# Performance work log

Measured on AMD Instinct MI355X. Metric: run time of the kernel, lower is better.

## Reference

```python
import jax, jax.numpy as jnp
import numpy as np

VMF_KAPPA = 30.0      # vMF concentration
THRESHOLD = 0.0       # vc_thresholds
OCC_LIKELY = 0.6      # occ_likely[0]
NUM_MIXTURES = 4
EPS_L1 = 1e-12        # torch F.normalize eps


def _l1_normalize(x, axis):
    n = jnp.sum(jnp.abs(x), axis=axis, keepdims=True)
    return x / jnp.maximum(n, EPS_L1)


def _crop_or_pad(mm, H, W):
    # center crop or zero-pad mix model spatial dims to (H, W); shapes are static
    _, _, hm, wm = mm.shape
    if hm < H:
        d1 = (H - hm) // 2
        mm = jnp.pad(mm, ((0, 0), (0, 0), (d1, H - hm - d1), (0, 0)))
    elif hm > H:
        d1 = (hm - H) // 2
        mm = mm[:, :, d1:d1 + H, :]
    if wm < W:
        d1 = (W - wm) // 2
        mm = jnp.pad(mm, ((0, 0), (0, 0), (0, 0), (d1, W - wm - d1)))
    elif wm > W:
        d1 = (wm - W) // 2
        mm = mm[:, :, :, d1:d1 + W]
    return mm


def setup_inputs() -> dict:
    key = jax.random.key(0)
    k1, k2, k3, k4 = jax.random.split(key, 4)
    B, C, H, W = 32, 512, 56, 56
    VC = 512              # number of vMF codebook vectors
    KM = 48               # num_classes(12) * num_mixtures(4)
    NCLUT = 5             # clutter models
    return {
        "vgg_feat": jax.random.normal(k1, (B, C, H, W), dtype=jnp.float32),
        "conv_weight": jax.random.normal(k2, (VC, C, 1, 1), dtype=jnp.float32),
        "mix_model": jax.random.uniform(k3, (KM, VC, H, W), dtype=jnp.float32),
        "clutter_model": jax.random.uniform(k4, (NCLUT, VC), dtype=jnp.float32),
    }


def reference(vgg_feat, conv_weight, mix_model, clutter_model):
    B, C, H, W = vgg_feat.shape
    # --- Conv1o1: cosine similarity between L2-normalized features and codebook ---
    xnorm = jnp.linalg.norm(vgg_feat, axis=1, keepdims=True)
    xnorm = xnorm + (xnorm == 0).astype(vgg_feat.dtype)  # avoid div-by-zero
    xn = vgg_feat / xnorm
    w = conv_weight[:, :, 0, 0]                           # (vc, C) 1x1 kernel
    wn = w / jnp.linalg.norm(w, axis=1, keepdims=True)
    cos = jnp.einsum('bchw,kc->bkhw', xn, wn)             # (B, vc, H, W)
    # --- vMF activation ---
    act = jnp.exp(VMF_KAPPA * cos) * (cos > THRESHOLD).astype(cos.dtype)
    # --- PointwiseInferenceLayer (vmf, use_mixture_bg=True) ---
    ck = _l1_normalize(jnp.clip(clutter_model, 0.0, 1.0), axis=1)  # (N, vc)
    bg = jnp.einsum('bkhw,nk->bnhw', act, ck)                      # (B, N, H, W)
    background = jnp.log(bg * OCC_LIKELY + 1e-10)
    background = jnp.max(background, axis=1, keepdims=True)        # (B, 1, H, W)
    background = background[:, None, None]                         # (B,1,1,1,H,W)

    mm = _l1_normalize(jnp.clip(mix_model, 0.0, 1.0), axis=1)      # (KM, vc, Hm, Wm)
    mm = _crop_or_pad(mm, H, W)
    fg = jnp.einsum('bkhw,mkhw->bmhw', act, mm)                    # (B, KM, H, W)
    foreground = jnp.log(fg * (1.0 - OCC_LIKELY) + 1e-10)
    num_classes = mm.shape[0] // NUM_MIXTURES
    foreground = foreground.reshape(B, num_classes, NUM_MIXTURES, 1, H, W)
    per_model = jnp.maximum(foreground, background).sum(axis=(-1, -2))  # (B,K,M,1)
    scores = per_model.max(axis=-1).max(axis=-1)                        # (B, K)
    mix_likeli = scores / (H * W)
    # SoftMaxTemp(2.0)
    z = jnp.exp(jnp.clip(mix_likeli * 2.0, -88.7, 88.7))
    soft = z / jnp.sum(z, axis=1, keepdims=True)
    return soft, vgg_feat, mix_likeli
```

## Files before the change

kernel.cpp:

```cpp
#include <hip/hip_runtime.h>

#define B_ 32
#define C_ 512
#define HW_ 3136
#define KF_ 512
#define KM_ 48
#define NCL_ 5

typedef __attribute__((ext_vector_type(8))) short short8;
typedef __attribute__((ext_vector_type(4))) short short4v;
typedef __attribute__((ext_vector_type(4))) float floatx4;
typedef unsigned int u32;
typedef u32 __attribute__((address_space(1))) gu32;
typedef u32 __attribute__((address_space(3))) lu32;

__device__ __forceinline__ unsigned short f2bf(float f) {
    union { float f; unsigned u; } v; v.f = f;
    unsigned r = v.u + 0x7FFFu + ((v.u >> 16) & 1u);
    return (unsigned short)(r >> 16);
}
__device__ __forceinline__ float bf2f(unsigned short u) {
    union { unsigned u; float f; } v; v.u = ((unsigned)u) << 16;
    return v.f;
}
__device__ __forceinline__ void gl2lds16(const void* g, void* l) {
    __builtin_amdgcn_global_load_lds((const gu32*)g, (lu32*)l, 16, 0, 0);
}
__device__ __forceinline__ void gl2lds4(const void* g, void* l) {
    __builtin_amdgcn_global_load_lds((const gu32*)g, (lu32*)l, 4, 0, 0);
}

__global__ __launch_bounds__(64) void prep_kernel(const float* __restrict__ w,
                                                  const float* __restrict__ cl,
                                                  unsigned short* __restrict__ wn,
                                                  unsigned short* __restrict__ ckb) {
    int bid = blockIdx.x, t = threadIdx.x;
    if (bid < KF_) {
        const float* row = w + (size_t)bid * C_;
        float ss = 0.f;
        float x[8];
#pragma unroll
        for (int j = 0; j < 8; ++j) { x[j] = row[t * 8 + j]; ss += x[j] * x[j]; }
        for (int m = 32; m >= 1; m >>= 1) ss += __shfl_xor(ss, m);
        float inv = 1.f / sqrtf(ss);
#pragma unroll
        for (int j = 0; j < 8; ++j) wn[(size_t)bid * C_ + t * 8 + j] = f2bf(x[j] * inv);
    } else {
        int n = bid - KF_;
        if (n >= 16) return;
        if (n < NCL_) {
            const float* row = cl + (size_t)n * KF_;
            float s = 0.f;
            float v[8];
#pragma unroll
            for (int j = 0; j < 8; ++j) {
                float x = row[t * 8 + j];
                x = fminf(fmaxf(x, 0.f), 1.f);
                v[j] = x; s += x;
            }
            for (int m = 32; m >= 1; m >>= 1) s += __shfl_xor(s, m);
            float inv = 1.f / fmaxf(s, 1e-12f);
#pragma unroll
            for (int j = 0; j < 8; ++j) ckb[(size_t)n * KF_ + t * 8 + j] = f2bf(v[j] * inv);
        } else {
#pragma unroll
            for (int j = 0; j < 8; ++j) ckb[(size_t)n * KF_ + t * 8 + j] = 0;
        }
    }
}

__global__ __launch_bounds__(512) void xprep_kernel(const float* __restrict__ vgg,
                                                    unsigned short* __restrict__ xnt,
                                                    float* __restrict__ invn,
                                                    float* __restrict__ out_vgg,
                                                    int write_vgg) {
    int pt = blockIdx.x, b = blockIdx.y;
    int tid = threadIdx.x;
    int px = tid & 63, cq = tid >> 6;
    __shared__ __align__(16) unsigned short tile[64][512];
    __shared__ float ssp[8][64];
    const float* vcol = vgg + (size_t)b * C_ * HW_ + pt * 64 + px;
    float* ovcol = out_vgg + (size_t)b * C_ * HW_ + pt * 64 + px;

    float ss = 0.f;
#pragma unroll
    for (int j = 0; j < 16; ++j) {
        int c0 = cq * 64 + j * 4;
        float x0 = vcol[(size_t)(c0 + 0) * HW_];
        float x1 = vcol[(size_t)(c0 + 1) * HW_];
        float x2 = vcol[(size_t)(c0 + 2) * HW_];
        float x3 = vcol[(size_t)(c0 + 3) * HW_];
        ss += x0 * x0 + x1 * x1 + x2 * x2 + x3 * x3;
        short4v pk;
        pk[0] = (short)f2bf(x0); pk[1] = (short)f2bf(x1);
        pk[2] = (short)f2bf(x2); pk[3] = (short)f2bf(x3);
        *(short4v*)&tile[px][c0] = pk;
        if (write_vgg) {
            ovcol[(size_t)(c0 + 0) * HW_] = x0;
            ovcol[(size_t)(c0 + 1) * HW_] = x1;
            ovcol[(size_t)(c0 + 2) * HW_] = x2;
            ovcol[(size_t)(c0 + 3) * HW_] = x3;
        }
    }
    ssp[cq][px] = ss;
    __syncthreads();
    if (tid < 64) {
        float s = 0.f;
#pragma unroll
        for (int q = 0; q < 8; ++q) s += ssp[q][tid];
        float n = sqrtf(s);
        invn[(size_t)b * HW_ + pt * 64 + tid] = (n == 0.f) ? 1.f : 1.f / n;
    }
    __syncthreads();
    int row = tid >> 3, ch = tid & 7;
    unsigned short* orow = xnt + ((size_t)b * HW_ + pt * 64 + row) * 512;
#pragma unroll
    for (int j = 0; j < 8; ++j) {
        int c8 = (ch + 8 * j) * 8;
        *(short8*)(orow + c8) = *(const short8*)&tile[row][c8];
    }
}

__global__ __launch_bounds__(512) void gemm_act_kernel(const unsigned short* __restrict__ xnt,
                                                       const unsigned short* __restrict__ wn,
                                                       const float* __restrict__ invn,
                                                       unsigned short* __restrict__ act) {
    int wg = blockIdx.x;
    int swz = (wg & 7) * 392 + (wg >> 3);
    int pt = swz >> 2, ft = swz & 3;
    int tid = threadIdx.x, lane = tid & 63;
    int wid = tid >> 6;
    int li = lane & 15, q = lane >> 4;
    int wm = wid & 1, wq = wid >> 1;

    __shared__ __align__(16) unsigned short a_lds[2][128 * 64];
    __shared__ __align__(16) unsigned short b_lds[2][128 * 64];
    __shared__ float inv_l[128];
    if (tid < 128) inv_l[tid] = invn[(size_t)pt * 128 + tid];

    const unsigned short* ga = wn + ((size_t)ft * 128 + (tid >> 3)) * 512 + (tid & 7) * 8;
    const unsigned short* gb = xnt + ((size_t)pt * 128 + (tid >> 3)) * 512 + (tid & 7) * 8;
    int ldst = tid * 8;

    floatx4 acc[4][2] = {};

#pragma unroll
    for (int i = 0; i < 2; ++i) {
        gl2lds16(ga + (size_t)i * 64 * 512, &a_lds[0][ldst + i * 4096]);
        gl2lds16(gb + (size_t)i * 64 * 512, &b_lds[0][ldst + i * 4096]);
    }
    __syncthreads();

#pragma unroll 1
    for (int s = 0; s < 8; ++s) {
        if (s < 7) {
            int nb = (s + 1) & 1;
#pragma unroll
            for (int i = 0; i < 2; ++i) {
                gl2lds16(ga + (size_t)i * 64 * 512 + (s + 1) * 64, &a_lds[nb][ldst + i * 4096]);
                gl2lds16(gb + (size_t)i * 64 * 512 + (s + 1) * 64, &b_lds[nb][ldst + i * 4096]);
            }
        }
        int buf = s & 1;
#pragma unroll
        for (int k2 = 0; k2 < 2; ++k2) {
            short8 af[4], bfr[2];
#pragma unroll
            for (int i = 0; i < 4; ++i)
                af[i] = *(const short8*)&a_lds[buf][(wm * 64 + i * 16 + li) * 64 + k2 * 32 + q * 8];
#pragma unroll
            for (int j = 0; j < 2; ++j)
                bfr[j] = *(const short8*)&b_lds[buf][(wq * 32 + j * 16 + li) * 64 + k2 * 32 + q * 8];
#pragma unroll
            for (int i = 0; i < 4; ++i)
#pragma unroll
                for (int j = 0; j < 2; ++j)
                    acc[i][j] = __builtin_amdgcn_mfma_f32_16x16x32_bf16(af[i], bfr[j], acc[i][j], 0, 0, 0);
        }
        __syncthreads();
    }

#pragma unroll
    for (int j = 0; j < 2; ++j) {
        int px = wq * 32 + j * 16 + li;
        float inv = inv_l[px];
        size_t row_g = (size_t)pt * 128 + px;
#pragma unroll
        for (int i = 0; i < 4; ++i) {
            int chn = ft * 8 + wm * 4 + i;
            short4v pk;
#pragma unroll
            for (int r = 0; r < 4; ++r) {
                float cv = acc[i][j][r] * inv;
                float a = cv > 0.f ? __expf(30.f * cv) : 0.f;
                pk[r] = (short)f2bf(a);
            }
            *(short4v*)(act + ((size_t)chn * 100352 + row_g) * 16 + q * 4) = pk;
        }
    }
}

#define MMBUF 50112
#define ACTBUF 16640
#define OFF_ACT0 (2*MMBUF)
#define OFF_CSUM (2*MMBUF + 2*ACTBUF)
#define OFF_PMS  (OFF_CSUM + 3072)
#define OFF_CKB  (OFF_PMS + 6144)
__global__ __launch_bounds__(1024) void fg_kernel(const unsigned short* __restrict__ act,
                                                  const float* __restrict__ mm,
                                                  const unsigned short* __restrict__ ckb,
                                                  float* __restrict__ pm) {
    __shared__ __align__(16) unsigned char L[OFF_CKB + 16 * 520 * 2];
    float* csum_s = (float*)(L + OFF_CSUM);
    float* pms    = (float*)(L + OFF_PMS);
    unsigned short* ckbl = (unsigned short*)(L + OFF_CKB);

    int p0 = blockIdx.x * 16;
    int tid = threadIdx.x;
    int lane = tid & 63, wid = tid >> 6;
    int li = lane & 15, q = lane >> 4;
    int pp = wid;
    int w3 = wid * 3;

    for (int i = tid; i < 1536; i += 1024) pms[i] = 0.f;
    {
        int row = tid >> 6, cg = tid & 63;
        *(short8*)&ckbl[row * 520 + cg * 8] = *(const short8*)(ckb + row * 512 + cg * 8);
    }

    const float* mm_src = mm + ((size_t)(w3 * KF_) + (size_t)(lane >> 4)) * HW_ + p0 + (lane & 15);
    const unsigned short* act_src = act +
        ((size_t)(2 * wid + (lane >> 5)) * HW_ + p0 + ((lane >> 1) & 15)) * 16 + (lane & 1) * 8;

    auto stage = [&](int s) {
        unsigned char* mb = L + (s & 1) * MMBUF;
        unsigned char* ab = L + OFF_ACT0 + (s & 1) * ACTBUF;
        const float* ms = mm_src + (size_t)s * 16 * HW_;
#pragma unroll
        for (int jj = 0; jj < 12; ++jj)
            gl2lds4(ms + (size_t)((jj >> 2) * KF_ + (jj & 3) * 4) * HW_,
                    mb + (w3 + (jj >> 2)) * 1044 + (jj & 3) * 256);
        gl2lds16(act_src + (size_t)s * 100352 * 16, ab + wid * 1040);
    };

    short8 fa[2] = {};
    short8 fmA[3] = {};
    short8 fck = {};
    floatx4 acc[3][2] = {};
    floatx4 accbg[2] = {};
    float csp[3] = {0.f, 0.f, 0.f};

    stage(0);
    __syncthreads();

#pragma unroll 2
    for (int s = 0; s < 32; ++s) {
        if (s < 31) stage(s + 1);
        const unsigned char* mc = L + (s & 1) * MMBUF;
        const unsigned char* ac = L + OFF_ACT0 + (s & 1) * ACTBUF;
        if ((q >> 1) == (s & 1)) {
#pragma unroll
            for (int bf = 0; bf < 2; ++bf)
                fa[bf] = *(const short8*)(ac + (bf * 8 + (li >> 1)) * 1040 +
                                          ((li & 1) * 16 + pp) * 32 + (q & 1) * 16);
#pragma unroll
            for (int mf = 0; mf < 3; ++mf) {
                const unsigned char* arow = mc + (mf * 16 + li) * 1044 + (q & 1) * 512 + pp * 4;
                short8 pk;
                float s0 = 0.f;
#pragma unroll
                for (int j = 0; j < 8; ++j) {
                    float x = *(const float*)(arow + j * 64);
                    x = fminf(fmaxf(x, 0.f), 1.f);
                    s0 += x;
                    pk[j] = (short)f2bf(x);
                }
                csp[mf] += s0;
                fmA[mf] = pk;
            }
            fck = *(const short8*)&ckbl[li * 520 + s * 16 + (q & 1) * 8];
        }
        if (s & 1) {
#pragma unroll
            for (int mf = 0; mf < 3; ++mf) {
                acc[mf][0] = __builtin_amdgcn_mfma_f32_16x16x32_bf16(fmA[mf], fa[0], acc[mf][0], 0, 0, 0);
                acc[mf][1] = __builtin_amdgcn_mfma_f32_16x16x32_bf16(fmA[mf], fa[1], acc[mf][1], 0, 0, 0);
            }
            accbg[0] = __builtin_amdgcn_mfma_f32_16x16x32_bf16(fck, fa[0], accbg[0], 0, 0, 0);
            accbg[1] = __builtin_amdgcn_mfma_f32_16x16x32_bf16(fck, fa[1], accbg[1], 0, 0, 0);
        }
        __syncthreads();
    }

#pragma unroll
    for (int mf = 0; mf < 3; ++mf) {
        float v = csp[mf];
        v += __shfl_xor(v, 16);
        v += __shfl_xor(v, 32);
        if (q == 0) csum_s[(mf * 16 + li) * 16 + pp] = v;
    }

    float bgv[2];
#pragma unroll
    for (int bf = 0; bf < 2; ++bf) {
        float v = -1e30f;
#pragma unroll
        for (int r = 0; r < 4; ++r) v = fmaxf(v, logf(accbg[bf][r] * 0.6f + 1e-10f));
        v = fmaxf(v, __shfl_xor(v, 16));
        v = fmaxf(v, __shfl_xor(v, 32));
        bgv[bf] = v;
    }
    __syncthreads();

#pragma unroll
    for (int mf = 0; mf < 3; ++mf)
#pragma unroll
        for (int bf = 0; bf < 2; ++bf) {
            int b = bf * 16 + li;
#pragma unroll
            for (int r = 0; r < 4; ++r) {
                int m = mf * 16 + q * 4 + r;
                float inv = 1.f / fmaxf(csum_s[m * 16 + pp], 1e-12f);
                float v = fmaxf(logf(acc[mf][bf][r] * inv * 0.4f + 1e-10f), bgv[bf]);
                atomicAdd(&pms[m * 32 + b], v);
            }
        }
    __syncthreads();
    if (tid < 512) {
        int i3 = tid * 3;
#pragma unroll
        for (int j = 0; j < 3; ++j) {
            int i = i3 + j;
            int m = i >> 5, b = i & 31;
            atomicAdd(&pm[(size_t)b * KM_ + m], pms[i]);
        }
    }
}

__global__ __launch_bounds__(64) void final_kernel(const float* __restrict__ pm,
                                                   float* __restrict__ out_soft,
                                                   float* __restrict__ out_ml) {
    int b = threadIdx.x;
    if (b >= B_) return;
    float ml[12];
#pragma unroll
    for (int c = 0; c < 12; ++c) {
        float s = -1e30f;
#pragma unroll
        for (int j = 0; j < 4; ++j) s = fmaxf(s, pm[(size_t)b * KM_ + c * 4 + j]);
        ml[c] = s / (float)HW_;
    }
    float z[12], zs = 0.f;
#pragma unroll
    for (int c = 0; c < 12; ++c) {
        float e = fminf(fmaxf(ml[c] * 2.f, -88.7f), 88.7f);
        z[c] = expf(e); zs += z[c];
    }
#pragma unroll
    for (int c = 0; c < 12; ++c) {
        out_soft[(size_t)b * 12 + c] = z[c] / zs;
        out_ml[(size_t)b * 12 + c] = ml[c];
    }
}

extern "C" void kernel_launch(void* const* d_in, const int* in_sizes, int n_in,
                              void* d_out, int out_size, void* d_ws, size_t ws_size,
                              hipStream_t stream) {
    const float* vgg = (const float*)d_in[0];
    const float* cw  = (const float*)d_in[1];
    const float* mmp = (const float*)d_in[2];
    const float* cl  = (const float*)d_in[3];
    float* out = (float*)d_out;
    char* ws = (char*)d_ws;

    unsigned short* wn   = (unsigned short*)(ws);
    unsigned short* ckb  = (unsigned short*)(ws + 524288);
    float* invn          = (float*)(ws + 540672);
    float* pm            = (float*)(ws + 942080);
    unsigned short* xnt  = (unsigned short*)(ws + 948224);
    const size_t ACT_OFF = 948224 + 102760448;
    const size_t ACT_BYTES = (size_t)B_ * HW_ * KF_ * 2;

    int big_ws = (ws_size >= ACT_OFF + ACT_BYTES) ? 1 : 0;
    unsigned short* act = big_ws ? (unsigned short*)(ws + ACT_OFF)
                                 : (unsigned short*)(out + 384);

    hipMemsetAsync(pm, 0, (size_t)B_ * KM_ * sizeof(float), stream);
    prep_kernel<<<dim3(KF_ + 16), dim3(64), 0, stream>>>(cw, cl, wn, ckb);
    xprep_kernel<<<dim3(49, 32), dim3(512), 0, stream>>>(vgg, xnt, invn, out + 384, big_ws);
    gemm_act_kernel<<<dim3(3136), dim3(512), 0, stream>>>(xnt, wn, invn, act);
    fg_kernel<<<dim3(196), dim3(1024), 0, stream>>>(act, mmp, ckb, pm);
    final_kernel<<<1, 64, 0, stream>>>(pm, out, out + 384 + (size_t)B_ * C_ * HW_);
    if (!big_ws)
        hipMemcpyAsync(out + 384, vgg, (size_t)B_ * C_ * HW_ * sizeof(float),
                       hipMemcpyDeviceToDevice, stream);
}
```

Baseline: 405.9 us.

## Pre-convert mix model to bf16 and add triple-buffered foreground MFMA kernel

Adds a prep kernel that clamps the fp32 mix model, converts it to bf16 in a blocked layout, and writes per-pixel channel sums. A new 512-thread foreground kernel consumes this with a 3-stage async global-to-LDS pipeline and explicit vmcnt waits. It replaces the old kernel, which read and normalized fp32 mix-model data inline. The GEMM kernel also swaps __syncthreads for raw barriers with partial vmcnt waits so loads overlap compute. The new path needs a much larger workspace and falls back to the old path if that is not available.

After: 448.1 us. 1.1x slower.

```diff
diff --git a/kernel.cpp b/kernel.cpp
--- a/kernel.cpp
+++ b/kernel.cpp
@@ -121,6 +121,36 @@
     }
 }
 
+__global__ __launch_bounds__(448) void mmprep_kernel(const float* __restrict__ mm,
+                                                     unsigned short* __restrict__ mmb,
+                                                     float* __restrict__ csumg) {
+    int m = blockIdx.x;
+    int kh = blockIdx.z;
+    int px = blockIdx.y * 448 + threadIdx.x;
+    const float* src = mm + ((size_t)m * KF_ + kh * 256) * HW_ + px;
+    unsigned short* dst = mmb + ((size_t)(m * 32 + kh * 16) * HW_ + px) * 16;
+    float cs = 0.f;
+#pragma unroll 1
+    for (int ch = 0; ch < 16; ++ch) {
+        short8 lo, hi;
+#pragma unroll
+        for (int kin = 0; kin < 8; ++kin) {
+            float x = src[(size_t)(ch * 16 + kin) * HW_];
+            x = fminf(fmaxf(x, 0.f), 1.f);
+            cs += x; lo[kin] = (short)f2bf(x);
+        }
+#pragma unroll
+        for (int kin = 8; kin < 16; ++kin) {
+            float x = src[(size_t)(ch * 16 + kin) * HW_];
+            x = fminf(fmaxf(x, 0.f), 1.f);
+            cs += x; hi[kin - 8] = (short)f2bf(x);
+        }
+        *(short8*)(dst + (size_t)ch * HW_ * 16) = lo;
+        *(short8*)(dst + (size_t)ch * HW_ * 16 + 8) = hi;
+    }
+    csumg[(size_t)kh * 48 * HW_ + (size_t)m * HW_ + px] = cs;
+}
+
 __global__ __launch_bounds__(512) void gemm_act_kernel(const unsigned short* __restrict__ xnt,
                                                        const unsigned short* __restrict__ wn,
                                                        const float* __restrict__ invn,
@@ -149,10 +179,10 @@
         gl2lds16(ga + (size_t)i * 64 * 512, &a_lds[0][ldst + i * 4096]);
         gl2lds16(gb + (size_t)i * 64 * 512, &b_lds[0][ldst + i * 4096]);
     }
-    __syncthreads();
 
 #pragma unroll 1
     for (int s = 0; s < 8; ++s) {
+        __builtin_amdgcn_s_barrier();
         if (s < 7) {
             int nb = (s + 1) & 1;
 #pragma unroll
@@ -160,7 +190,12 @@
                 gl2lds16(ga + (size_t)i * 64 * 512 + (s + 1) * 64, &a_lds[nb][ldst + i * 4096]);
                 gl2lds16(gb + (size_t)i * 64 * 512 + (s + 1) * 64, &b_lds[nb][ldst + i * 4096]);
             }
-        }
+            asm volatile("s_waitcnt vmcnt(4)" ::: "memory");
+        } else {
+            asm volatile("s_waitcnt vmcnt(0)" ::: "memory");
+        }
+        __builtin_amdgcn_sched_barrier(0);
+        __builtin_amdgcn_s_barrier();
         int buf = s & 1;
 #pragma unroll
         for (int k2 = 0; k2 < 2; ++k2) {
@@ -177,7 +212,6 @@
                 for (int j = 0; j < 2; ++j)
                     acc[i][j] = __builtin_amdgcn_mfma_f32_16x16x32_bf16(af[i], bfr[j], acc[i][j], 0, 0, 0);
         }
-        __syncthreads();
     }
 
 #pragma unroll
@@ -196,6 +230,148 @@
                 pk[r] = (short)f2bf(a);
             }
             *(short4v*)(act + ((size_t)chn * 100352 + row_g) * 16 + q * 4) = pk;
+        }
+    }
+}
+
+#define FG_ABUF 16640
+#define FG_MBUF 24960
+#define FG_BUF  (FG_ABUF + FG_MBUF)
+#define FG_OFF_CSUM (3 * FG_BUF)
+#define FG_OFF_PMS  (FG_OFF_CSUM + 3072)
+#define FG_OFF_CKB  (FG_OFF_PMS + 6144)
+__global__ __launch_bounds__(512) void fg2_kernel(const unsigned short* __restrict__ act,
+                                                  const unsigned short* __restrict__ mmb,
+                                                  const float* __restrict__ csumg,
+                                                  const unsigned short* __restrict__ ckb,
+                                                  float* __restrict__ pm) {
+    __shared__ __align__(16) unsigned char L[150656];
+    float* csum_s = (float*)(L + FG_OFF_CSUM);
+    float* pms    = (float*)(L + FG_OFF_PMS);
+    unsigned short* ckbl = (unsigned short*)(L + FG_OFF_CKB);
+
+    int p0 = blockIdx.x * 16;
+    int tid = threadIdx.x;
+    int lane = tid & 63, w = tid >> 6;
+    int li = lane & 15, q = lane >> 4;
+
+    for (int i = tid; i < 1536; i += 512) pms[i] = 0.f;
+    for (int i = tid; i < 768; i += 512) {
+        int m = i >> 4, pp = i & 15;
+        size_t idx = (size_t)m * HW_ + p0 + pp;
+        csum_s[i] = csumg[idx] + csumg[(size_t)48 * HW_ + idx];
+    }
+    {
+        int row = tid >> 5, cg = tid & 31;
+        *(short8*)&ckbl[row * 520 + cg * 16] = *(const short8*)(ckb + row * 512 + cg * 16);
+        *(short8*)&ckbl[row * 520 + cg * 16 + 8] = *(const short8*)(ckb + row * 512 + cg * 16 + 8);
+    }
+    __syncthreads();
+
+    size_t a_lane = ((size_t)(lane >> 5) * HW_ + p0 + ((lane >> 1) & 15)) * 16 + (lane & 1) * 8;
+    size_t m_lane = (size_t)(lane >> 5) * 1605632 + ((size_t)p0 + ((lane >> 1) & 15)) * 16 + (lane & 1) * 8;
+
+    auto stage = [&](int s) {
+        unsigned char* ab = L + (s % 3) * FG_BUF;
+        unsigned char* mb = ab + FG_ABUF;
+        const unsigned short* as = act + (size_t)s * 1605632 + a_lane;
+        const unsigned short* ms = mmb + (size_t)s * 50176 + m_lane;
+#pragma unroll
+        for (int t = 0; t < 2; ++t) {
+            int j = w + t * 8;
+            gl2lds16(as + (size_t)(2 * j) * (HW_ * 16), ab + j * 1040);
+        }
+#pragma unroll
+        for (int t = 0; t < 3; ++t) {
+            int j = w + t * 8;
+            gl2lds16(ms + (size_t)(2 * j) * 1605632, mb + j * 1040);
+        }
+    };
+
+    short8 fa[2][2] = {};
+    short8 fm[2][3] = {};
+    short8 fck = {};
+    floatx4 acc[2][3][2] = {};
+    floatx4 abg[2][2] = {};
+
+    stage(0);
+    stage(1);
+
+#pragma unroll 2
+    for (int s = 0; s < 32; ++s) {
+        __builtin_amdgcn_s_barrier();
+        if (s < 30) {
+            stage(s + 2);
+            asm volatile("s_waitcnt vmcnt(10)" ::: "memory");
+        } else if (s == 30) {
+            asm volatile("s_waitcnt vmcnt(5)" ::: "memory");
+        } else {
+            asm volatile("s_waitcnt vmcnt(0)" ::: "memory");
+        }
+        __builtin_amdgcn_sched_barrier(0);
+        __builtin_amdgcn_s_barrier();
+        const unsigned char* ab = L + (s % 3) * FG_BUF;
+        const unsigned char* mb = ab + FG_ABUF;
+        if ((q >> 1) == (s & 1)) {
+#pragma unroll
+            for (int e = 0; e < 2; ++e) {
+                int pp = w * 2 + e;
+#pragma unroll
+                for (int bf = 0; bf < 2; ++bf)
+                    fa[e][bf] = *(const short8*)(ab + (bf * 8 + (li >> 1)) * 1040 +
+                                                 ((li & 1) * 16 + pp) * 32 + (q & 1) * 16);
+#pragma unroll
+                for (int mf = 0; mf < 3; ++mf)
+                    fm[e][mf] = *(const short8*)(mb + (mf * 8 + (li >> 1)) * 1040 +
+                                                 ((li & 1) * 16 + pp) * 32 + (q & 1) * 16);
+            }
+            fck = *(const short8*)&ckbl[li * 520 + s * 16 + (q & 1) * 8];
+        }
+        if (s & 1) {
+#pragma unroll
+            for (int e = 0; e < 2; ++e) {
+#pragma unroll
+                for (int mf = 0; mf < 3; ++mf) {
+                    acc[e][mf][0] = __builtin_amdgcn_mfma_f32_16x16x32_bf16(fm[e][mf], fa[e][0], acc[e][mf][0], 0, 0, 0);
+                    acc[e][mf][1] = __builtin_amdgcn_mfma_f32_16x16x32_bf16(fm[e][mf], fa[e][1], acc[e][mf][1], 0, 0, 0);
+                }
+                abg[e][0] = __builtin_amdgcn_mfma_f32_16x16x32_bf16(fck, fa[e][0], abg[e][0], 0, 0, 0);
+                abg[e][1] = __builtin_amdgcn_mfma_f32_16x16x32_bf16(fck, fa[e][1], abg[e][1], 0, 0, 0);
+            }
+        }
+    }
+
+#pragma unroll
+    for (int e = 0; e < 2; ++e) {
+        int pp = w * 2 + e;
+#pragma unroll
+        for (int bf = 0; bf < 2; ++bf) {
+            int b = bf * 16 + li;
+            float v = -1e30f;
+#pragma unroll
+            for (int r = 0; r < 4; ++r) v = fmaxf(v, logf(abg[e][bf][r] * 0.6f + 1e-10f));
+            v = fmaxf(v, __shfl_xor(v, 16));
+            v = fmaxf(v, __shfl_xor(v, 32));
+            float bgv = v;
+#pragma unroll
+            for (int mf = 0; mf < 3; ++mf)
+#pragma unroll
+                for (int r = 0; r < 4; ++r) {
+                    int m = mf * 16 + q * 4 + r;
+                    float inv = 1.f / fmaxf(csum_s[m * 16 + pp], 1e-12f);
+                    float fv = fmaxf(logf(acc[e][mf][bf][r] * inv * 0.4f + 1e-10f), bgv);
+                    atomicAdd(&pms[m * 32 + b], fv);
+                }
+        }
+    }
+    __syncthreads();
+    {
+        int i3 = tid * 3;
+#pragma unroll
+        for (int j = 0; j < 3; ++j) {
+            int i = i3 + j;
+            int m = i >> 5, b = i & 31;
+            atomicAdd(&pm[(size_t)b * KM_ + m], pms[i]);
         }
     }
 }
@@ -206,10 +382,10 @@
 #define OFF_CSUM (2*MMBUF + 2*ACTBUF)
 #define OFF_PMS  (OFF_CSUM + 3072)
 #define OFF_CKB  (OFF_PMS + 6144)
-__global__ __launch_bounds__(1024) void fg_kernel(const unsigned short* __restrict__ act,
-                                                  const float* __restrict__ mm,
-                                                  const unsigned short* __restrict__ ckb,
-                                                  float* __restrict__ pm) {
+__global__ __launch_bounds__(1024) void fg_fb_kernel(const unsigned short* __restrict__ act,
+                                                     const float* __restrict__ mm,
+                                                     const unsigned short* __restrict__ ckb,
+                                                     float* __restrict__ pm) {
     __shared__ __align__(16) unsigned char L[OFF_CKB + 16 * 520 * 2];
     float* csum_s = (float*)(L + OFF_CSUM);
     float* pms    = (float*)(L + OFF_PMS);
@@ -377,21 +553,39 @@
     unsigned short* ckb  = (unsigned short*)(ws + 524288);
     float* invn          = (float*)(ws + 540672);
     float* pm            = (float*)(ws + 942080);
-    unsigned short* xnt  = (unsigned short*)(ws + 948224);
-    const size_t ACT_OFF = 948224 + 102760448;
+    float* csumg         = (float*)(ws + 948224);
+    unsigned short* xnt  = (unsigned short*)(ws + 2152448);
+    unsigned short* mmb  = (unsigned short*)(ws + 104912896);
+    const size_t MID_NEED = 104912896ull + 154140672ull;
     const size_t ACT_BYTES = (size_t)B_ * HW_ * KF_ * 2;
-
-    int big_ws = (ws_size >= ACT_OFF + ACT_BYTES) ? 1 : 0;
-    unsigned short* act = big_ws ? (unsigned short*)(ws + ACT_OFF)
-                                 : (unsigned short*)(out + 384);
 
     hipMemsetAsync(pm, 0, (size_t)B_ * KM_ * sizeof(float), stream);
     prep_kernel<<<dim3(KF_ + 16), dim3(64), 0, stream>>>(cw, cl, wn, ckb);
-    xprep_kernel<<<dim3(49, 32), dim3(512), 0, stream>>>(vgg, xnt, invn, out + 384, big_ws);
-    gemm_act_kernel<<<dim3(3136), dim3(512), 0, stream>>>(xnt, wn, invn, act);
-    fg_kernel<<<dim3(196), dim3(1024), 0, stream>>>(act, mmp, ckb, pm);
-    final_kernel<<<1, 64, 0, stream>>>(pm, out, out + 384 + (size_t)B_ * C_ * HW_);
-    if (!big_ws)
-        hipMemcpyAsync(out + 384, vgg, (size_t)B_ * C_ * HW_ * sizeof(float),
-                       hipMemcpyDeviceToDevice, stream);
-}
+
+    if (ws_size >= MID_NEED) {
+        int act_in_ws = (ws_size >= MID_NEED + ACT_BYTES) ? 1 : 0;
+        unsigned short* act = act_in_ws ? (unsigned short*)(ws + MID_NEED)
+                                        : (unsigned short*)(out + 384);
+        xprep_kernel<<<dim3(49, 32), dim3(512), 0, stream>>>(vgg, xnt, invn, out + 384, act_in_ws);
+        mmprep_kernel<<<dim3(48, 7, 2), dim3(448), 0, stream>>>(mmp, mmb, csumg);
+        gemm_act_kernel<<<dim3(3136), dim3(512), 0, stream>>>(xnt, wn, invn, act);
+        fg2_kernel<<<dim3(196), dim3(512), 0, stream>>>(act, mmb, csumg, ckb, pm);
+        final_kernel<<<1, 64, 0, stream>>>(pm, out, out + 384 + (size_t)B_ * C_ * HW_);
+        if (!act_in_ws)
+            hipMemcpyAsync(out + 384, vgg, (size_t)B_ * C_ * HW_ * sizeof(float),
+                           hipMemcpyDeviceToDevice, stream);
+    } else {
+        unsigned short* xnt2 = (unsigned short*)(ws + 948224);
+        const size_t ACT_OFF = 948224 + 102760448;
+        int big_ws = (ws_size >= ACT_OFF + ACT_BYTES) ? 1 : 0;
+        unsigned short* act = big_ws ? (unsigned short*)(ws + ACT_OFF)
+                                     : (unsigned short*)(out + 384);
+        xprep_kernel<<<dim3(49, 32), dim3(512), 0, stream>>>(vgg, xnt2, invn, out + 384, big_ws);
+        gemm_act_kernel<<<dim3(3136), dim3(512), 0, stream>>>(xnt2, wn, invn, act);
+        fg_fb_kernel<<<dim3(196), dim3(1024), 0, stream>>>(act, mmp, ckb, pm);
+        final_kernel<<<1, 64, 0, stream>>>(pm, out, out + 384 + (size_t)B_ * C_ * HW_);
+        if (!big_ws)
+            hipMemcpyAsync(out + 384, vgg, (size_t)B_ * C_ * HW_ * sizeof(float),
+                           hipMemcpyDeviceToDevice, stream);
+    }
+}
```

## Fuse background clutter reduction into GEMM epilogue and retile foreground kernel

Applied to the files above, without the earlier changes.

Moves the clutter-model background dot product into the GEMM epilogue, accumulating per-pixel fp32 sums through shared-memory and global atomics into a new workspace buffer. This removes the background MFMA work from the foreground kernel. The foreground kernel is rewritten as fg3 with 64-pixel by 16-mixture tiles, XOR-swizzled LDS layouts and a 4-step register staging cycle. The GEMM main loop replaces __syncthreads with explicit vmcnt waits and split barriers. The cost is an extra memset, extra global atomics per pixel, and higher LDS use in the GEMM.

Result: slower. 451.9 us (+11.3%).

```diff
diff --git a/kernel.cpp b/kernel.cpp
--- a/kernel.cpp
+++ b/kernel.cpp
@@ -19,21 +19,14 @@
     unsigned r = v.u + 0x7FFFu + ((v.u >> 16) & 1u);
     return (unsigned short)(r >> 16);
 }
-__device__ __forceinline__ float bf2f(unsigned short u) {
-    union { unsigned u; float f; } v; v.u = ((unsigned)u) << 16;
-    return v.f;
-}
 __device__ __forceinline__ void gl2lds16(const void* g, void* l) {
     __builtin_amdgcn_global_load_lds((const gu32*)g, (lu32*)l, 16, 0, 0);
-}
-__device__ __forceinline__ void gl2lds4(const void* g, void* l) {
-    __builtin_amdgcn_global_load_lds((const gu32*)g, (lu32*)l, 4, 0, 0);
 }
 
 __global__ __launch_bounds__(64) void prep_kernel(const float* __restrict__ w,
                                                   const float* __restrict__ cl,
                                                   unsigned short* __restrict__ wn,
-                                                  unsigned short* __restrict__ ckb) {
+                                                  float* __restrict__ ck) {
     int bid = blockIdx.x, t = threadIdx.x;
     if (bid < KF_) {
         const float* row = w + (size_t)bid * C_;
@@ -47,25 +40,20 @@
         for (int j = 0; j < 8; ++j) wn[(size_t)bid * C_ + t * 8 + j] = f2bf(x[j] * inv);
     } else {
         int n = bid - KF_;
-        if (n >= 16) return;
-        if (n < NCL_) {
-            const float* row = cl + (size_t)n * KF_;
-            float s = 0.f;
-            float v[8];
-#pragma unroll
-            for (int j = 0; j < 8; ++j) {
-                float x = row[t * 8 + j];
-                x = fminf(fmaxf(x, 0.f), 1.f);
-                v[j] = x; s += x;
-            }
-            for (int m = 32; m >= 1; m >>= 1) s += __shfl_xor(s, m);
-            float inv = 1.f / fmaxf(s, 1e-12f);
-#pragma unroll
-            for (int j = 0; j < 8; ++j) ckb[(size_t)n * KF_ + t * 8 + j] = f2bf(v[j] * inv);
-        } else {
-#pragma unroll
-            for (int j = 0; j < 8; ++j) ckb[(size_t)n * KF_ + t * 8 + j] = 0;
-        }
+        if (n >= NCL_) return;
+        const float* row = cl + (size_t)n * KF_;
+        float s = 0.f;
+        float v[8];
+#pragma unroll
+        for (int j = 0; j < 8; ++j) {
+            float x = row[t * 8 + j];
+            x = fminf(fmaxf(x, 0.f), 1.f);
+            v[j] = x; s += x;
+        }
+        for (int m = 32; m >= 1; m >>= 1) s += __shfl_xor(s, m);
+        float inv = 1.f / fmaxf(s, 1e-12f);
+#pragma unroll
+        for (int j = 0; j < 8; ++j) ck[(size_t)n * KF_ + t * 8 + j] = v[j] * inv;
     }
 }
 
@@ -124,7 +112,9 @@
 __global__ __launch_bounds__(512) void gemm_act_kernel(const unsigned short* __restrict__ xnt,
                                                        const unsigned short* __restrict__ wn,
                                                        const float* __restrict__ invn,
-                                                       unsigned short* __restrict__ act) {
+                                                       const float* __restrict__ ck,
+                                                       unsigned short* __restrict__ act,
+                                                       float* __restrict__ bgacc) {
     int wg = blockIdx.x;
     int swz = (wg & 7) * 392 + (wg >> 3);
     int pt = swz >> 2, ft = swz & 3;
@@ -136,7 +126,11 @@
     __shared__ __align__(16) unsigned short a_lds[2][128 * 64];
     __shared__ __align__(16) unsigned short b_lds[2][128 * 64];
     __shared__ float inv_l[128];
+    __shared__ float ck_l[NCL_ * KF_];
+    __shared__ float bga_l[128 * NCL_];
     if (tid < 128) inv_l[tid] = invn[(size_t)pt * 128 + tid];
+    for (int i = tid; i < NCL_ * KF_; i += 512) ck_l[i] = ck[i];
+    for (int i = tid; i < 128 * NCL_; i += 512) bga_l[i] = 0.f;
 
     const unsigned short* ga = wn + ((size_t)ft * 128 + (tid >> 3)) * 512 + (tid & 7) * 8;
     const unsigned short* gb = xnt + ((size_t)pt * 128 + (tid >> 3)) * 512 + (tid & 7) * 8;
@@ -149,10 +143,10 @@
         gl2lds16(ga + (size_t)i * 64 * 512, &a_lds[0][ldst + i * 4096]);
         gl2lds16(gb + (size_t)i * 64 * 512, &b_lds[0][ldst + i * 4096]);
     }
-    __syncthreads();
 
 #pragma unroll 1
     for (int s = 0; s < 8; ++s) {
+        __builtin_amdgcn_s_barrier();
         if (s < 7) {
             int nb = (s + 1) & 1;
 #pragma unroll
@@ -160,7 +154,12 @@
                 gl2lds16(ga + (size_t)i * 64 * 512 + (s + 1) * 64, &a_lds[nb][ldst + i * 4096]);
                 gl2lds16(gb + (size_t)i * 64 * 512 + (s + 1) * 64, &b_lds[nb][ldst + i * 4096]);
             }
-        }
+            asm volatile("s_waitcnt vmcnt(4)" ::: "memory");
+        } else {
+            asm volatile("s_waitcnt vmcnt(0)" ::: "memory");
+        }
+        __builtin_amdgcn_sched_barrier(0);
+        __builtin_amdgcn_s_barrier();
         int buf = s & 1;
 #pragma unroll
         for (int k2 = 0; k2 < 2; ++k2) {
@@ -177,7 +176,6 @@
                 for (int j = 0; j < 2; ++j)
                     acc[i][j] = __builtin_amdgcn_mfma_f32_16x16x32_bf16(af[i], bfr[j], acc[i][j], 0, 0, 0);
         }
-        __syncthreads();
     }
 
 #pragma unroll
@@ -185,155 +183,189 @@
         int px = wq * 32 + j * 16 + li;
         float inv = inv_l[px];
         size_t row_g = (size_t)pt * 128 + px;
+        float bp[NCL_] = {0.f, 0.f, 0.f, 0.f, 0.f};
 #pragma unroll
         for (int i = 0; i < 4; ++i) {
             int chn = ft * 8 + wm * 4 + i;
+            int f_g = ft * 128 + wm * 64 + i * 16 + q * 4;
             short4v pk;
+            float av[4];
 #pragma unroll
             for (int r = 0; r < 4; ++r) {
                 float cv = acc[i][j][r] * inv;
                 float a = cv > 0.f ? __expf(30.f * cv) : 0.f;
+                av[r] = a;
                 pk[r] = (short)f2bf(a);
             }
             *(short4v*)(act + ((size_t)chn * 100352 + row_g) * 16 + q * 4) = pk;
-        }
-    }
-}
-
-#define MMBUF 50112
-#define ACTBUF 16640
-#define OFF_ACT0 (2*MMBUF)
-#define OFF_CSUM (2*MMBUF + 2*ACTBUF)
-#define OFF_PMS  (OFF_CSUM + 3072)
-#define OFF_CKB  (OFF_PMS + 6144)
-__global__ __launch_bounds__(1024) void fg_kernel(const unsigned short* __restrict__ act,
+#pragma unroll
+            for (int n = 0; n < NCL_; ++n)
+                bp[n] += av[0] * ck_l[n * KF_ + f_g] + av[1] * ck_l[n * KF_ + f_g + 1] +
+                         av[2] * ck_l[n * KF_ + f_g + 2] + av[3] * ck_l[n * KF_ + f_g + 3];
+        }
+#pragma unroll
+        for (int n = 0; n < NCL_; ++n) {
+            float v = bp[n];
+            v += __shfl_xor(v, 16);
+            v += __shfl_xor(v, 32);
+            if (q == 0) atomicAdd(&bga_l[px * NCL_ + n], v);
+        }
+    }
+    __syncthreads();
+    if (tid < 128) {
+        size_t row_g = (size_t)pt * 128 + tid;
+#pragma unroll
+        for (int n = 0; n < NCL_; ++n)
+            atomicAdd(&bgacc[row_g * 8 + n], bga_l[tid * NCL_ + n]);
+    }
+}
+
+__global__ __launch_bounds__(512) void fg3_kernel(const unsigned short* __restrict__ act,
                                                   const float* __restrict__ mm,
-                                                  const unsigned short* __restrict__ ckb,
+                                                  const float* __restrict__ bgacc,
                                                   float* __restrict__ pm) {
-    __shared__ __align__(16) unsigned char L[OFF_CKB + 16 * 520 * 2];
-    float* csum_s = (float*)(L + OFF_CSUM);
-    float* pms    = (float*)(L + OFF_PMS);
-    unsigned short* ckbl = (unsigned short*)(L + OFF_CKB);
-
-    int p0 = blockIdx.x * 16;
+    __shared__ __align__(16) unsigned char L[145408];
+    float* bgs    = (float*)(L + 131072);
+    float* csum_s = (float*)(L + 139264);
+    float* pms    = (float*)(L + 143360);
+
+    int bid = blockIdx.x;
+    int xcd = bid & 7, rest = bid >> 3;
+    int mg = rest % 3, ptq = rest / 3;
+    int pt = xcd + 8 * ptq;
+    if (pt >= 49) return;
+    int px0 = pt * 64;
+    int m0 = mg * 16;
+
     int tid = threadIdx.x;
-    int lane = tid & 63, wid = tid >> 6;
+    int lane = tid & 63, w = tid >> 6;
     int li = lane & 15, q = lane >> 4;
-    int pp = wid;
-    int w3 = wid * 3;
-
-    for (int i = tid; i < 1536; i += 1024) pms[i] = 0.f;
-    {
-        int row = tid >> 6, cg = tid & 63;
-        *(short8*)&ckbl[row * 520 + cg * 8] = *(const short8*)(ckb + row * 512 + cg * 8);
-    }
-
-    const float* mm_src = mm + ((size_t)(w3 * KF_) + (size_t)(lane >> 4)) * HW_ + p0 + (lane & 15);
-    const unsigned short* act_src = act +
-        ((size_t)(2 * wid + (lane >> 5)) * HW_ + p0 + ((lane >> 1) & 15)) * 16 + (lane & 1) * 8;
+    int w8 = w * 8;
+
+    pms[tid & 511] = 0.f;
+    for (int i = tid; i < 2048; i += 512) {
+        int b = i >> 6, p = i & 63;
+        const float* bgp = bgacc + ((size_t)b * HW_ + px0 + p) * 8;
+        float mx = -1e30f;
+#pragma unroll
+        for (int n = 0; n < NCL_; ++n) mx = fmaxf(mx, logf(bgp[n] * 0.6f + 1e-10f));
+        bgs[i] = mx;
+    }
+
+    const unsigned short* srcA[4];
+    int dA[4];
+#pragma unroll
+    for (int t = 0; t < 4; ++t) {
+        int b = w * 4 + t;
+        srcA[t] = act + ((size_t)b * HW_ + px0 + (lane ^ (b & 7))) * 16;
+        dA[t] = b * 1024 + lane * 16;
+    }
+    const float* srcM[2][2];
+    int dM[2][2];
+#pragma unroll
+    for (int u = 0; u < 2; ++u)
+#pragma unroll
+        for (int kq = 0; kq < 2; ++kq) {
+            int m = w * 2 + u;
+            int k = kq * 4 + (lane >> 4);
+            int g = (lane & 15) ^ m;
+            srcM[u][kq] = mm + ((size_t)(m0 + m) * KF_ + k) * HW_ + px0 + g * 4;
+            dM[u][kq] = m * 2048 + kq * 1024 + lane * 16;
+        }
 
     auto stage = [&](int s) {
-        unsigned char* mb = L + (s & 1) * MMBUF;
-        unsigned char* ab = L + OFF_ACT0 + (s & 1) * ACTBUF;
-        const float* ms = mm_src + (size_t)s * 16 * HW_;
-#pragma unroll
-        for (int jj = 0; jj < 12; ++jj)
-            gl2lds4(ms + (size_t)((jj >> 2) * KF_ + (jj & 3) * 4) * HW_,
-                    mb + (w3 + (jj >> 2)) * 1044 + (jj & 3) * 256);
-        gl2lds16(act_src + (size_t)s * 100352 * 16, ab + wid * 1040);
+        unsigned char* base = L + (size_t)(s & 1) * 65536;
+#pragma unroll
+        for (int t = 0; t < 4; ++t)
+            gl2lds16(srcA[t] + (size_t)(s >> 1) * 1605632 + (s & 1) * 8, base + dA[t]);
+#pragma unroll
+        for (int u = 0; u < 2; ++u)
+#pragma unroll
+            for (int kq = 0; kq < 2; ++kq)
+                gl2lds16(srcM[u][kq] + (size_t)s * 8 * HW_, base + 32768 + dM[u][kq]);
     };
 
-    short8 fa[2] = {};
-    short8 fmA[3] = {};
-    short8 fck = {};
-    floatx4 acc[3][2] = {};
-    floatx4 accbg[2] = {};
-    float csp[3] = {0.f, 0.f, 0.f};
+    short8 fA[8], fb0[8], fb1[8];
+    floatx4 acc0[8] = {}, acc1[8] = {};
+    float csp[8] = {0.f, 0.f, 0.f, 0.f, 0.f, 0.f, 0.f, 0.f};
 
     stage(0);
-    __syncthreads();
-
-#pragma unroll 2
-    for (int s = 0; s < 32; ++s) {
-        if (s < 31) stage(s + 1);
-        const unsigned char* mc = L + (s & 1) * MMBUF;
-        const unsigned char* ac = L + OFF_ACT0 + (s & 1) * ACTBUF;
-        if ((q >> 1) == (s & 1)) {
-#pragma unroll
-            for (int bf = 0; bf < 2; ++bf)
-                fa[bf] = *(const short8*)(ac + (bf * 8 + (li >> 1)) * 1040 +
-                                          ((li & 1) * 16 + pp) * 32 + (q & 1) * 16);
-#pragma unroll
-            for (int mf = 0; mf < 3; ++mf) {
-                const unsigned char* arow = mc + (mf * 16 + li) * 1044 + (q & 1) * 512 + pp * 4;
+
+#pragma unroll 4
+    for (int s = 0; s < 64; ++s) {
+        __builtin_amdgcn_s_barrier();
+        if (s < 63) {
+            stage(s + 1);
+            asm volatile("s_waitcnt vmcnt(8)" ::: "memory");
+        } else {
+            asm volatile("s_waitcnt vmcnt(0)" ::: "memory");
+        }
+        __builtin_amdgcn_sched_barrier(0);
+        __builtin_amdgcn_s_barrier();
+        const unsigned char* ab = L + (size_t)(s & 1) * 65536;
+        const unsigned char* mb = ab + 32768;
+        int rq = s & 3;
+        if (q == rq) {
+#pragma unroll
+            for (int e = 0; e < 8; ++e) {
+                int p = w8 + e;
+                int slotA = (p ^ (li & 7)) * 16;
+                fb0[e] = *(const short8*)(ab + li * 1024 + slotA);
+                fb1[e] = *(const short8*)(ab + (16 + li) * 1024 + slotA);
+                const unsigned char* mrow = mb + li * 2048 +
+                                            ((((p >> 2) ^ li) & 15) * 16) + (p & 3) * 4;
                 short8 pk;
-                float s0 = 0.f;
-#pragma unroll
-                for (int j = 0; j < 8; ++j) {
-                    float x = *(const float*)(arow + j * 64);
+                float cs = 0.f;
+#pragma unroll
+                for (int k = 0; k < 8; ++k) {
+                    float x = *(const float*)(mrow + k * 256);
                     x = fminf(fmaxf(x, 0.f), 1.f);
-                    s0 += x;
-                    pk[j] = (short)f2bf(x);
+                    cs += x;
+                    pk[k] = (short)f2bf(x);
                 }
-                csp[mf] += s0;
-                fmA[mf] = pk;
+                csp[e] += cs;
+                fA[e] = pk;
             }
-            fck = *(const short8*)&ckbl[li * 520 + s * 16 + (q & 1) * 8];
-        }
-        if (s & 1) {
-#pragma unroll
-            for (int mf = 0; mf < 3; ++mf) {
-                acc[mf][0] = __builtin_amdgcn_mfma_f32_16x16x32_bf16(fmA[mf], fa[0], acc[mf][0], 0, 0, 0);
-                acc[mf][1] = __builtin_amdgcn_mfma_f32_16x16x32_bf16(fmA[mf], fa[1], acc[mf][1], 0, 0, 0);
+        }
+        if (rq == 3) {
+#pragma unroll
+            for (int e = 0; e < 8; ++e) {
+                acc0[e] = __builtin_amdgcn_mfma_f32_16x16x32_bf16(fA[e], fb0[e], acc0[e], 0, 0, 0);
+                acc1[e] = __builtin_amdgcn_mfma_f32_16x16x32_bf16(fA[e], fb1[e], acc1[e], 0, 0, 0);
             }
-            accbg[0] = __builtin_amdgcn_mfma_f32_16x16x32_bf16(fck, fa[0], accbg[0], 0, 0, 0);
-            accbg[1] = __builtin_amdgcn_mfma_f32_16x16x32_bf16(fck, fa[1], accbg[1], 0, 0, 0);
-        }
-        __syncthreads();
-    }
-
-#pragma unroll
-    for (int mf = 0; mf < 3; ++mf) {
-        float v = csp[mf];
+        }
+    }
+
+#pragma unroll
+    for (int e = 0; e < 8; ++e) {
+        float v = csp[e];
         v += __shfl_xor(v, 16);
         v += __shfl_xor(v, 32);
-        if (q == 0) csum_s[(mf * 16 + li) * 16 + pp] = v;
-    }
-
-    float bgv[2];
+        if (q == 0) csum_s[li * 64 + w8 + e] = v;
+    }
+    __syncthreads();
+
 #pragma unroll
     for (int bf = 0; bf < 2; ++bf) {
-        float v = -1e30f;
-#pragma unroll
-        for (int r = 0; r < 4; ++r) v = fmaxf(v, logf(accbg[bf][r] * 0.6f + 1e-10f));
-        v = fmaxf(v, __shfl_xor(v, 16));
-        v = fmaxf(v, __shfl_xor(v, 32));
-        bgv[bf] = v;
+        int b = bf * 16 + li;
+#pragma unroll
+        for (int r = 0; r < 4; ++r) {
+            int ml = q * 4 + r;
+            float sacc = 0.f;
+#pragma unroll
+            for (int e = 0; e < 8; ++e) {
+                int p = w8 + e;
+                float inv = 1.f / fmaxf(csum_s[ml * 64 + p], 1e-12f);
+                float a = (bf == 0) ? acc0[e][r] : acc1[e][r];
+                sacc += fmaxf(logf(a * inv * 0.4f + 1e-10f), bgs[b * 64 + p]);
+            }
+            atomicAdd(&pms[ml * 32 + b], sacc);
+        }
     }
     __syncthreads();
-
-#pragma unroll
-    for (int mf = 0; mf < 3; ++mf)
-#pragma unroll
-        for (int bf = 0; bf < 2; ++bf) {
-            int b = bf * 16 + li;
-#pragma unroll
-            for (int r = 0; r < 4; ++r) {
-                int m = mf * 16 + q * 4 + r;
-                float inv = 1.f / fmaxf(csum_s[m * 16 + pp], 1e-12f);
-                float v = fmaxf(logf(acc[mf][bf][r] * inv * 0.4f + 1e-10f), bgv[bf]);
-                atomicAdd(&pms[m * 32 + b], v);
-            }
-        }
-    __syncthreads();
-    if (tid < 512) {
-        int i3 = tid * 3;
-#pragma unroll
-        for (int j = 0; j < 3; ++j) {
-            int i = i3 + j;
-            int m = i >> 5, b = i & 31;
-            atomicAdd(&pm[(size_t)b * KM_ + m], pms[i]);
-        }
+    {
+        int ml = tid >> 5, b = tid & 31;
+        atomicAdd(&pm[(size_t)b * KM_ + m0 + ml], pms[tid]);
     }
 }
 
@@ -374,24 +406,26 @@
     char* ws = (char*)d_ws;
 
     unsigned short* wn   = (unsigned short*)(ws);
-    unsigned short* ckb  = (unsigned short*)(ws + 524288);
-    float* invn          = (float*)(ws + 540672);
-    float* pm            = (float*)(ws + 942080);
-    unsigned short* xnt  = (unsigned short*)(ws + 948224);
-    const size_t ACT_OFF = 948224 + 102760448;
+    float* ck            = (float*)(ws + 524288);
+    float* invn          = (float*)(ws + 534528);
+    float* pm            = (float*)(ws + 935936);
+    float* bgacc         = (float*)(ws + 942080);
+    unsigned short* xnt  = (unsigned short*)(ws + 4153344);
+    const size_t ACT_OFF = 4153344 + 102760448;
     const size_t ACT_BYTES = (size_t)B_ * HW_ * KF_ * 2;
 
-    int big_ws = (ws_size >= ACT_OFF + ACT_BYTES) ? 1 : 0;
-    unsigned short* act = big_ws ? (unsigned short*)(ws + ACT_OFF)
-                                 : (unsigned short*)(out + 384);
+    int act_in_ws = (ws_size >= ACT_OFF + ACT_BYTES) ? 1 : 0;
+    unsigned short* act = act_in_ws ? (unsigned short*)(ws + ACT_OFF)
+                                    : (unsigned short*)(out + 384);
 
     hipMemsetAsync(pm, 0, (size_t)B_ * KM_ * sizeof(float), stream);
-    prep_kernel<<<dim3(KF_ + 16), dim3(64), 0, stream>>>(cw, cl, wn, ckb);
-    xprep_kernel<<<dim3(49, 32), dim3(512), 0, stream>>>(vgg, xnt, invn, out + 384, big_ws);
-    gemm_act_kernel<<<dim3(3136), dim3(512), 0, stream>>>(xnt, wn, invn, act);
-    fg_kernel<<<dim3(196), dim3(1024), 0, stream>>>(act, mmp, ckb, pm);
+    hipMemsetAsync(bgacc, 0, (size_t)B_ * HW_ * 8 * sizeof(float), stream);
+    prep_kernel<<<dim3(KF_ + NCL_), dim3(64), 0, stream>>>(cw, cl, wn, ck);
+    xprep_kernel<<<dim3(49, 32), dim3(512), 0, stream>>>(vgg, xnt, invn, out + 384, act_in_ws);
+    gemm_act_kernel<<<dim3(3136), dim3(512), 0, stream>>>(xnt, wn, invn, ck, act, bgacc);
+    fg3_kernel<<<dim3(168), dim3(512), 0, stream>>>(act, mmp, bgacc, pm);
     final_kernel<<<1, 64, 0, stream>>>(pm, out, out + 384 + (size_t)B_ * C_ * HW_);
-    if (!big_ws)
+    if (!act_in_ws)
         hipMemcpyAsync(out + 384, vgg, (size_t)B_ * C_ * HW_ * sizeof(float),
                        hipMemcpyDeviceToDevice, stream);
 }
```
